# Optimization experiments

Hardware: AMD Instinct MI355X
Metric: run time of the kernel (lower is better)

Reference implementation:

```python
import jax, jax.numpy as jnp
import numpy as np
import math

B, T, C, H = 4, 2048, 768, 12
D = C // H  # 64 head dim

def setup_inputs() -> dict:
    key = jax.random.key(0)
    k1, k2, k3 = jax.random.split(key, 3)
    x = jax.random.normal(k1, (B, T, C), dtype=jnp.float32)
    mask = jnp.tril(jnp.ones((T, T), dtype=bool))[None, None, :, :]  # causal [1,1,T,T]
    W_attn = jax.random.normal(k2, (C, 3 * C), dtype=jnp.float32) * 0.02
    b_attn = jnp.zeros((3 * C,), dtype=jnp.float32)
    W_proj = jax.random.normal(k3, (C, C), dtype=jnp.float32) * (0.02 / math.sqrt(2 * 12))
    b_proj = jnp.zeros((C,), dtype=jnp.float32)
    return {"x": x, "mask": mask, "W_attn": W_attn, "b_attn": b_attn,
            "W_proj": W_proj, "b_proj": b_proj}

def reference(x, mask, W_attn, b_attn, W_proj, b_proj):
    Bx, Tx, Cx = x.shape
    qkv = x @ W_attn + b_attn                       # [B,T,3C]
    qkv = qkv.reshape(Bx, Tx, 3 * H, D).transpose(0, 2, 1, 3)  # [B,3H,T,D]
    q, k, v = jnp.array_split(qkv, 3, axis=1)       # each [B,H,T,D]
    att = jnp.einsum('bhqd,bhkd->bhqk', q, k) / math.sqrt(D)  # [B,H,T,T]
    att = jnp.where(mask == 0, -jnp.inf, att)
    att = jax.nn.softmax(att, axis=-1)
    y = jnp.einsum('bhqk,bhkd->bhqd', att, v)       # [B,H,T,D]
    y = y.transpose(0, 2, 1, 3).reshape(Bx, Tx, Cx)
    return y @ W_proj + b_proj
```

## Files before the change

kernel.cpp:

```cpp
#include <hip/hip_runtime.h>
#include <math.h>

#define BB 4
#define TT 2048
#define CC 768
#define HH 12
#define DD 64
#define RS (3 * CC)

typedef __bf16 bf16x8 __attribute__((ext_vector_type(8)));
typedef float f32x4 __attribute__((ext_vector_type(4)));
typedef unsigned short u16x8 __attribute__((ext_vector_type(8)));

union U8 { bf16x8 v; u16x8 s; unsigned short u[8]; };
union BCV { __bf16 h; unsigned short u; };

__device__ __forceinline__ unsigned short f2bf(float f) {
  union { float f; unsigned u; } x; x.f = f;
  unsigned r = x.u + 0x7fffu + ((x.u >> 16) & 1u);
  return (unsigned short)(r >> 16);
}

#define AS1 __attribute__((address_space(1)))
#define AS3 __attribute__((address_space(3)))
__device__ __forceinline__ void gl_lds16(const void* g, void* l) {
  __builtin_amdgcn_global_load_lds((const AS1 unsigned int*)g,
                                   (AS3 unsigned int*)l, 16, 0, 0);
}

__global__ __launch_bounds__(256) void cvt_bf16_kernel(
    const float* __restrict__ in, unsigned short* __restrict__ out, int n8) {
  int i = blockIdx.x * 256 + threadIdx.x;
  const int stride = gridDim.x * 256;
  for (; i < n8; i += stride) {
    const float4 a = reinterpret_cast<const float4*>(in)[i * 2];
    const float4 b = reinterpret_cast<const float4*>(in)[i * 2 + 1];
    U8 p;
    p.u[0] = f2bf(a.x); p.u[1] = f2bf(a.y); p.u[2] = f2bf(a.z); p.u[3] = f2bf(a.w);
    p.u[4] = f2bf(b.x); p.u[5] = f2bf(b.y); p.u[6] = f2bf(b.z); p.u[7] = f2bf(b.w);
    reinterpret_cast<u16x8*>(out)[i] = p.s;
  }
}

__global__ __launch_bounds__(256) void transpose_cvt_kernel(
    const float* __restrict__ in, unsigned short* __restrict__ out,
    int K, int N) {
  __shared__ float T[64][65];
  const int k0 = blockIdx.y * 64, n0 = blockIdx.x * 64;
  const int tid = threadIdx.x;
  const int ty = tid >> 4, tx4 = (tid & 15) * 4;
#pragma unroll
  for (int i = 0; i < 4; ++i) {
    const int r = ty + i * 16;
    const float4 v = *reinterpret_cast<const float4*>(
        &in[(size_t)(k0 + r) * N + n0 + tx4]);
    T[r][tx4] = v.x; T[r][tx4 + 1] = v.y; T[r][tx4 + 2] = v.z; T[r][tx4 + 3] = v.w;
  }
  __syncthreads();
  const int nrow = tid >> 2, kc = (tid & 3) * 16;
  U8 p0, p1;
#pragma unroll
  for (int i = 0; i < 8; ++i) {
    p0.u[i] = f2bf(T[kc + i][nrow]);
    p1.u[i] = f2bf(T[kc + 8 + i][nrow]);
  }
  unsigned short* o = &out[(size_t)(n0 + nrow) * K + k0 + kc];
  *reinterpret_cast<u16x8*>(o) = p0.s;
  *reinterpret_cast<u16x8*>(o + 8) = p1.s;
}

__global__ __launch_bounds__(256) void vtrans_kernel(
    const unsigned short* __restrict__ qkvb, unsigned short* __restrict__ Vg) {
  __shared__ unsigned short Tt[64][72];
  const int tok0 = blockIdx.x * 64;
  const int bh = blockIdx.y, b = bh / HH, h = bh % HH;
  const int tid = threadIdx.x;
  const int r = tid >> 2, c = (tid & 3) * 16;
  const unsigned short* src =
      qkvb + (size_t)(b * TT + tok0 + r) * RS + (2 * HH + h) * DD + c;
  *reinterpret_cast<u16x8*>(&Tt[r][c]) = *reinterpret_cast<const u16x8*>(src);
  *reinterpret_cast<u16x8*>(&Tt[r][c + 8]) =
      *reinterpret_cast<const u16x8*>(src + 8);
  __syncthreads();
  const int d = tid >> 2, tc = (tid & 3) * 16;
  U8 o0, o1;
#pragma unroll
  for (int i = 0; i < 8; ++i) {
    o0.u[i] = Tt[tc + i][d];
    o1.u[i] = Tt[tc + 8 + i][d];
  }
  unsigned short* dst = Vg + ((size_t)bh * DD + d) * TT + tok0 + tc;
  *reinterpret_cast<u16x8*>(dst) = o0.s;
  *reinterpret_cast<u16x8*>(dst + 8) = o1.s;
}

template <typename OutT>
__global__ __launch_bounds__(256) void gemm_mfma_kernel(
    const unsigned short* __restrict__ A, const unsigned short* __restrict__ Bt,
    const float* __restrict__ bias, OutT* __restrict__ C,
    int M, int N, int K) {
  __shared__ unsigned short As[128 * 32];
  __shared__ unsigned short Bs[128 * 32];

  const int tid = threadIdx.x;
  const int w = tid >> 6, l = tid & 63, lr = l & 15, lg = l >> 4;
  const int wr = w >> 1, wc = w & 1;
  const int brow = blockIdx.y * 128, bcol = blockIdx.x * 128;

  f32x4 acc[4][4];
#pragma unroll
  for (int i = 0; i < 4; ++i)
#pragma unroll
    for (int j = 0; j < 4; ++j) acc[i][j] = (f32x4)(0.f);

  const int r0 = tid >> 2, c8 = (tid & 3) * 8;
  const unsigned short* gA = A + (size_t)(brow + r0) * K + c8;
  const unsigned short* gB = Bt + (size_t)(bcol + r0) * K + c8;
  unsigned short* lA = As + w * 512;
  unsigned short* lB = Bs + w * 512;

  for (int k0 = 0; k0 < K; k0 += 32) {
    __syncthreads();
    gl_lds16(gA + k0, lA);
    gl_lds16(gA + (size_t)64 * K + k0, lA + 2048);
    gl_lds16(gB + k0, lB);
    gl_lds16(gB + (size_t)64 * K + k0, lB + 2048);
    __syncthreads();

    bf16x8 af[4], bf[4];
#pragma unroll
    for (int mf = 0; mf < 4; ++mf)
      af[mf] = *reinterpret_cast<const bf16x8*>(
          &As[(wr * 64 + mf * 16 + lr) * 32 + lg * 8]);
#pragma unroll
    for (int nf = 0; nf < 4; ++nf)
      bf[nf] = *reinterpret_cast<const bf16x8*>(
          &Bs[(wc * 64 + nf * 16 + lr) * 32 + lg * 8]);
#pragma unroll
    for (int mf = 0; mf < 4; ++mf)
#pragma unroll
      for (int nf = 0; nf < 4; ++nf)
        acc[mf][nf] = __builtin_amdgcn_mfma_f32_16x16x32_bf16(
            af[mf], bf[nf], acc[mf][nf], 0, 0, 0);
  }

#pragma unroll
  for (int nf = 0; nf < 4; ++nf) {
    const int col = bcol + wc * 64 + nf * 16 + lr;
    const float bv = bias[col];
#pragma unroll
    for (int mf = 0; mf < 4; ++mf) {
      const int row0 = brow + wr * 64 + mf * 16 + lg * 4;
#pragma unroll
      for (int r = 0; r < 4; ++r) {
        const float v = acc[mf][nf][r] + bv;
        if constexpr (sizeof(OutT) == 2)
          C[(size_t)(row0 + r) * N + col] = (OutT)f2bf(v);
        else
          C[(size_t)(row0 + r) * N + col] = (OutT)v;
      }
    }
  }
}

constexpr int KVT = 64;

__global__ __launch_bounds__(256) void attn_mfma_kernel(
    const unsigned short* __restrict__ qkv,
    const unsigned short* __restrict__ Vg,
    unsigned short* __restrict__ y) {
  __shared__ unsigned short Ks[KVT * 64];
  __shared__ unsigned short Vt[DD * 64];
  __shared__ unsigned short Pl[4 * 16 * 64];

  const int tid = threadIdx.x;
  const int w = tid >> 6, l = tid & 63;
  const int lr = l & 15, lg = l >> 4;
  const int bh = blockIdx.x, b = bh / HH, h = bh % HH;
  const int g = 31 - blockIdx.y;
  const int qw = g * 64 + w * 16;

  const unsigned short* qbase = qkv + (size_t)b * TT * RS + h * DD;
  const unsigned short* kbase = qkv + (size_t)b * TT * RS + (HH + h) * DD;
  const unsigned short* vgb = Vg + (size_t)bh * DD * TT;

  const float qscale = 0.125f * 1.44269504f;
  const int e = lg ^ (lr & 7);
  const int e4 = e ^ 4;

  bf16x8 qf[2];
  {
    const unsigned short* qrow = qbase + (size_t)(qw + lr) * RS;
    qf[0] = *reinterpret_cast<const bf16x8*>(qrow + lg * 8);
    qf[1] = *reinterpret_cast<const bf16x8*>(qrow + lg * 8 + 32);
  }

  f32x4 O[4];
  f32x4 ls = (f32x4)(0.f);
#pragma unroll
  for (int nb = 0; nb < 4; ++nb) O[nb] = (f32x4)(0.f);

  const int srow = tid >> 2, sc2 = (tid & 3) * 2;
  const int sw = srow & 7;
  const int sidx0 = srow * 64 + 8 * (sc2 ^ sw);
  const int sidx1 = srow * 64 + 8 * ((sc2 + 1) ^ sw);
  const int scol = (tid & 3) * 16;
  const unsigned short* kptr = kbase + (size_t)srow * RS + scol;
  const unsigned short* vptr = vgb + (size_t)srow * TT + scol;

  const int ntiles = g + 1;
  u16x8 kr0 = *reinterpret_cast<const u16x8*>(kptr);
  u16x8 kr1 = *reinterpret_cast<const u16x8*>(kptr + 8);
  u16x8 vr0 = *reinterpret_cast<const u16x8*>(vptr);
  u16x8 vr1 = *reinterpret_cast<const u16x8*>(vptr + 8);

  for (int t = 0; t < ntiles; ++t) {
    const int kv0 = t * KVT;
    __syncthreads();
    *reinterpret_cast<u16x8*>(&Ks[sidx0]) = kr0;
    *reinterpret_cast<u16x8*>(&Ks[sidx1]) = kr1;
    *reinterpret_cast<u16x8*>(&Vt[sidx0]) = vr0;
    *reinterpret_cast<u16x8*>(&Vt[sidx1]) = vr1;
    if (t + 1 < ntiles) {
      kptr += (size_t)KVT * RS;
      vptr += KVT;
      kr0 = *reinterpret_cast<const u16x8*>(kptr);
      kr1 = *reinterpret_cast<const u16x8*>(kptr + 8);
      vr0 = *reinterpret_cast<const u16x8*>(vptr);
      vr1 = *reinterpret_cast<const u16x8*>(vptr + 8);
    }
    __syncthreads();

    const bool diag = (t == g);
    const int nbmax = diag ? (w + 1) : 4;

    f32x4 s[4];
#pragma unroll
    for (int nb = 0; nb < 4; ++nb) s[nb] = (f32x4)(0.f);
#pragma unroll
    for (int nb = 0; nb < 4; ++nb) {
      if (nb >= nbmax) continue;
      const int krow = (nb * 16 + lr) * 64;
      const bf16x8 k0 = *reinterpret_cast<const bf16x8*>(&Ks[krow + 8 * e]);
      const bf16x8 k1 = *reinterpret_cast<const bf16x8*>(&Ks[krow + 8 * e4]);
      s[nb] = __builtin_amdgcn_mfma_f32_16x16x32_bf16(qf[0], k0, s[nb], 0, 0, 0);
      s[nb] = __builtin_amdgcn_mfma_f32_16x16x32_bf16(qf[1], k1, s[nb], 0, 0, 0);
    }

#pragma unroll
    for (int nb = 0; nb < 4; ++nb)
#pragma unroll
      for (int r = 0; r < 4; ++r) s[nb][r] *= qscale;
    if (diag) {
      const int qrow = qw + lg * 4;
#pragma unroll
      for (int nb = 0; nb < 4; ++nb) {
        const int key = kv0 + nb * 16 + lr;
#pragma unroll
        for (int r = 0; r < 4; ++r)
          if (key > qrow + r) s[nb][r] = -1e30f;
      }
    }
#pragma unroll
    for (int r = 0; r < 4; ++r) {
      const int prow = lg * 4 + r;
      const int pswz = (prow & 7) << 3;
      unsigned short* pbase = &Pl[w * 1024 + prow * 64];
#pragma unroll
      for (int nb = 0; nb < 4; ++nb) {
        const float p = exp2f(s[nb][r]);
        ls[r] += p;
        BCV cv; cv.h = (__bf16)p;
        pbase[(nb * 16 + lr) ^ pswz] = cv.u;
      }
    }

    asm volatile("s_waitcnt lgkmcnt(0)" ::: "memory");

    {
      const unsigned short* pw = &Pl[w * 1024];
      const bf16x8 pa0 = *reinterpret_cast<const bf16x8*>(&pw[lr * 64 + 8 * e]);
      const bf16x8 pa1 = *reinterpret_cast<const bf16x8*>(&pw[lr * 64 + 8 * e4]);
#pragma unroll
      for (int nb = 0; nb < 4; ++nb) {
        const int vrow = (nb * 16 + lr) * 64;
        const bf16x8 v0 = *reinterpret_cast<const bf16x8*>(&Vt[vrow + 8 * e]);
        const bf16x8 v1 = *reinterpret_cast<const bf16x8*>(&Vt[vrow + 8 * e4]);
        O[nb] = __builtin_amdgcn_mfma_f32_16x16x32_bf16(pa0, v0, O[nb], 0, 0, 0);
        O[nb] = __builtin_amdgcn_mfma_f32_16x16x32_bf16(pa1, v1, O[nb], 0, 0, 0);
      }
    }
  }

#pragma unroll
  for (int off = 1; off < 16; off <<= 1)
#pragma unroll
    for (int r = 0; r < 4; ++r) ls[r] += __shfl_xor(ls[r], off, 64);
  f32x4 inv;
#pragma unroll
  for (int r = 0; r < 4; ++r) inv[r] = 1.f / ls[r];
#pragma unroll
  for (int nb = 0; nb < 4; ++nb)
#pragma unroll
    for (int r = 0; r < 4; ++r)
      y[((size_t)b * TT + qw + lg * 4 + r) * CC + h * DD + nb * 16 + lr] =
          f2bf(O[nb][r] * inv[r]);
}

extern "C" void kernel_launch(void* const* d_in, const int* in_sizes, int n_in,
                              void* d_out, int out_size, void* d_ws, size_t ws_size,
                              hipStream_t stream) {
  const float* x      = (const float*)d_in[0];
  const float* W_attn = (const float*)d_in[2];
  const float* b_attn = (const float*)d_in[3];
  const float* W_proj = (const float*)d_in[4];
  const float* b_proj = (const float*)d_in[5];
  float* out = (float*)d_out;

  const int M = BB * TT;
  unsigned short* qkvb = (unsigned short*)d_ws;
  unsigned short* xb   = qkvb + (size_t)M * RS;
  unsigned short* yb   = xb + (size_t)M * CC;
  unsigned short* Wt1  = yb + (size_t)M * CC;
  unsigned short* Wt2  = Wt1 + (size_t)RS * CC;
  unsigned short* Vg   = xb;

  cvt_bf16_kernel<<<1024, 256, 0, stream>>>(x, xb, M * CC / 8);
  transpose_cvt_kernel<<<dim3(RS / 64, CC / 64), 256, 0, stream>>>(
      W_attn, Wt1, CC, RS);
  transpose_cvt_kernel<<<dim3(CC / 64, CC / 64), 256, 0, stream>>>(
      W_proj, Wt2, CC, CC);

  gemm_mfma_kernel<unsigned short><<<dim3(RS / 128, M / 128), 256, 0, stream>>>(
      xb, Wt1, b_attn, qkvb, M, RS, CC);

  vtrans_kernel<<<dim3(TT / 64, BB * HH), 256, 0, stream>>>(qkvb, Vg);

  attn_mfma_kernel<<<dim3(BB * HH, 32), 256, 0, stream>>>(qkvb, Vg, yb);

  gemm_mfma_kernel<float><<<dim3(CC / 128, M / 128), 256, 0, stream>>>(
      yb, Wt2, b_proj, out, M, CC, CC);
}
```

Measured before the change: 154.5 us.

## Double-buffer LDS tiles in GEMM and attention kernels, one barrier per iteration

Both the GEMM and the attention kernel now use two LDS buffers. The next K/V or A/B tile is written into the spare buffer while MFMAs consume the current one, which cuts the barriers per loop iteration from two to one. The aim is to overlap global-to-LDS staging with compute and reduce synchronisation stalls. The cost is double the LDS footprint, which may lower occupancy.

```diff
diff --git a/kernel.cpp b/kernel.cpp
--- a/kernel.cpp
+++ b/kernel.cpp
@@ -99,8 +99,8 @@
     const unsigned short* __restrict__ A, const unsigned short* __restrict__ Bt,
     const float* __restrict__ bias, OutT* __restrict__ C,
     int M, int N, int K) {
-  __shared__ unsigned short As[128 * 32];
-  __shared__ unsigned short Bs[128 * 32];
+  __shared__ unsigned short As[2][128 * 32];
+  __shared__ unsigned short Bs[2][128 * 32];
 
   const int tid = threadIdx.x;
   const int w = tid >> 6, l = tid & 63, lr = l & 15, lg = l >> 4;
@@ -116,32 +116,41 @@
   const int r0 = tid >> 2, c8 = (tid & 3) * 8;
   const unsigned short* gA = A + (size_t)(brow + r0) * K + c8;
   const unsigned short* gB = Bt + (size_t)(bcol + r0) * K + c8;
-  unsigned short* lA = As + w * 512;
-  unsigned short* lB = Bs + w * 512;
-
+
+  gl_lds16(gA, As[0] + w * 512);
+  gl_lds16(gA + (size_t)64 * K, As[0] + w * 512 + 2048);
+  gl_lds16(gB, Bs[0] + w * 512);
+  gl_lds16(gB + (size_t)64 * K, Bs[0] + w * 512 + 2048);
+  __syncthreads();
+
+  int cur = 0;
   for (int k0 = 0; k0 < K; k0 += 32) {
-    __syncthreads();
-    gl_lds16(gA + k0, lA);
-    gl_lds16(gA + (size_t)64 * K + k0, lA + 2048);
-    gl_lds16(gB + k0, lB);
-    gl_lds16(gB + (size_t)64 * K + k0, lB + 2048);
-    __syncthreads();
+    if (k0 + 32 < K) {
+      const int kn = k0 + 32;
+      gl_lds16(gA + kn, As[cur ^ 1] + w * 512);
+      gl_lds16(gA + (size_t)64 * K + kn, As[cur ^ 1] + w * 512 + 2048);
+      gl_lds16(gB + kn, Bs[cur ^ 1] + w * 512);
+      gl_lds16(gB + (size_t)64 * K + kn, Bs[cur ^ 1] + w * 512 + 2048);
+    }
 
     bf16x8 af[4], bf[4];
 #pragma unroll
     for (int mf = 0; mf < 4; ++mf)
       af[mf] = *reinterpret_cast<const bf16x8*>(
-          &As[(wr * 64 + mf * 16 + lr) * 32 + lg * 8]);
+          &As[cur][(wr * 64 + mf * 16 + lr) * 32 + lg * 8]);
 #pragma unroll
     for (int nf = 0; nf < 4; ++nf)
       bf[nf] = *reinterpret_cast<const bf16x8*>(
-          &Bs[(wc * 64 + nf * 16 + lr) * 32 + lg * 8]);
+          &Bs[cur][(wc * 64 + nf * 16 + lr) * 32 + lg * 8]);
 #pragma unroll
     for (int mf = 0; mf < 4; ++mf)
 #pragma unroll
       for (int nf = 0; nf < 4; ++nf)
         acc[mf][nf] = __builtin_amdgcn_mfma_f32_16x16x32_bf16(
             af[mf], bf[nf], acc[mf][nf], 0, 0, 0);
+
+    __syncthreads();
+    cur ^= 1;
   }
 
 #pragma unroll
@@ -169,8 +178,8 @@
     const unsigned short* __restrict__ qkv,
     const unsigned short* __restrict__ Vg,
     unsigned short* __restrict__ y) {
-  __shared__ unsigned short Ks[KVT * 64];
-  __shared__ unsigned short Vt[DD * 64];
+  __shared__ unsigned short Ks[2][KVT * 64];
+  __shared__ unsigned short Vt[2][DD * 64];
   __shared__ unsigned short Pl[4 * 16 * 64];
 
   const int tid = threadIdx.x;
@@ -214,22 +223,38 @@
   u16x8 vr0 = *reinterpret_cast<const u16x8*>(vptr);
   u16x8 vr1 = *reinterpret_cast<const u16x8*>(vptr + 8);
 
+  *reinterpret_cast<u16x8*>(&Ks[0][sidx0]) = kr0;
+  *reinterpret_cast<u16x8*>(&Ks[0][sidx1]) = kr1;
+  *reinterpret_cast<u16x8*>(&Vt[0][sidx0]) = vr0;
+  *reinterpret_cast<u16x8*>(&Vt[0][sidx1]) = vr1;
+  if (ntiles > 1) {
+    kptr += (size_t)KVT * RS;
+    vptr += KVT;
+    kr0 = *reinterpret_cast<const u16x8*>(kptr);
+    kr1 = *reinterpret_cast<const u16x8*>(kptr + 8);
+    vr0 = *reinterpret_cast<const u16x8*>(vptr);
+    vr1 = *reinterpret_cast<const u16x8*>(vptr + 8);
+  }
+  __syncthreads();
+
+  int cur = 0;
   for (int t = 0; t < ntiles; ++t) {
     const int kv0 = t * KVT;
-    __syncthreads();
-    *reinterpret_cast<u16x8*>(&Ks[sidx0]) = kr0;
-    *reinterpret_cast<u16x8*>(&Ks[sidx1]) = kr1;
-    *reinterpret_cast<u16x8*>(&Vt[sidx0]) = vr0;
-    *reinterpret_cast<u16x8*>(&Vt[sidx1]) = vr1;
+
     if (t + 1 < ntiles) {
-      kptr += (size_t)KVT * RS;
-      vptr += KVT;
-      kr0 = *reinterpret_cast<const u16x8*>(kptr);
-      kr1 = *reinterpret_cast<const u16x8*>(kptr + 8);
-      vr0 = *reinterpret_cast<const u16x8*>(vptr);
-      vr1 = *reinterpret_cast<const u16x8*>(vptr + 8);
-    }
-    __syncthreads();
+      *reinterpret_cast<u16x8*>(&Ks[cur ^ 1][sidx0]) = kr0;
+      *reinterpret_cast<u16x8*>(&Ks[cur ^ 1][sidx1]) = kr1;
+      *reinterpret_cast<u16x8*>(&Vt[cur ^ 1][sidx0]) = vr0;
+      *reinterpret_cast<u16x8*>(&Vt[cur ^ 1][sidx1]) = vr1;
+      if (t + 2 < ntiles) {
+        kptr += (size_t)KVT * RS;
+        vptr += KVT;
+        kr0 = *reinterpret_cast<const u16x8*>(kptr);
+        kr1 = *reinterpret_cast<const u16x8*>(kptr + 8);
+        vr0 = *reinterpret_cast<const u16x8*>(vptr);
+        vr1 = *reinterpret_cast<const u16x8*>(vptr + 8);
+      }
+    }
 
     const bool diag = (t == g);
     const int nbmax = diag ? (w + 1) : 4;
@@ -241,8 +266,8 @@
     for (int nb = 0; nb < 4; ++nb) {
       if (nb >= nbmax) continue;
       const int krow = (nb * 16 + lr) * 64;
-      const bf16x8 k0 = *reinterpret_cast<const bf16x8*>(&Ks[krow + 8 * e]);
-      const bf16x8 k1 = *reinterpret_cast<const bf16x8*>(&Ks[krow + 8 * e4]);
+      const bf16x8 k0 = *reinterpret_cast<const bf16x8*>(&Ks[cur][krow + 8 * e]);
+      const bf16x8 k1 = *reinterpret_cast<const bf16x8*>(&Ks[cur][krow + 8 * e4]);
       s[nb] = __builtin_amdgcn_mfma_f32_16x16x32_bf16(qf[0], k0, s[nb], 0, 0, 0);
       s[nb] = __builtin_amdgcn_mfma_f32_16x16x32_bf16(qf[1], k1, s[nb], 0, 0, 0);
     }
@@ -284,12 +309,15 @@
 #pragma unroll
       for (int nb = 0; nb < 4; ++nb) {
         const int vrow = (nb * 16 + lr) * 64;
-        const bf16x8 v0 = *reinterpret_cast<const bf16x8*>(&Vt[vrow + 8 * e]);
-        const bf16x8 v1 = *reinterpret_cast<const bf16x8*>(&Vt[vrow + 8 * e4]);
+        const bf16x8 v0 = *reinterpret_cast<const bf16x8*>(&Vt[cur][vrow + 8 * e]);
+        const bf16x8 v1 = *reinterpret_cast<const bf16x8*>(&Vt[cur][vrow + 8 * e4]);
         O[nb] = __builtin_amdgcn_mfma_f32_16x16x32_bf16(pa0, v0, O[nb], 0, 0, 0);
         O[nb] = __builtin_amdgcn_mfma_f32_16x16x32_bf16(pa1, v1, O[nb], 0, 0, 0);
       }
     }
+
+    __syncthreads();
+    cur ^= 1;
   }
 
 #pragma unroll
```

Result: slower. 158.2 us (+2.4%).

## Double-buffer GEMM LDS tiles and trim masked softmax work in attention

Applied to the files above, without the earlier changes.

The GEMM kernel now keeps two LDS buffers and issues the global-to-LDS loads for the next K slice before running the MFMAs on the current one, so each iteration needs one barrier instead of two. In the attention kernel the qscale multiply is folded into the exp2 argument and masked-out key blocks on the diagonal tile skip exp2, writing zeros instead. s_setprio raises wave priority around the MFMA sections. LDS use in the GEMM doubles, which can lower occupancy.

```diff
diff --git a/kernel.cpp b/kernel.cpp
--- a/kernel.cpp
+++ b/kernel.cpp
@@ -99,8 +99,8 @@
     const unsigned short* __restrict__ A, const unsigned short* __restrict__ Bt,
     const float* __restrict__ bias, OutT* __restrict__ C,
     int M, int N, int K) {
-  __shared__ unsigned short As[128 * 32];
-  __shared__ unsigned short Bs[128 * 32];
+  __shared__ unsigned short As[2][128 * 32];
+  __shared__ unsigned short Bs[2][128 * 32];
 
   const int tid = threadIdx.x;
   const int w = tid >> 6, l = tid & 63, lr = l & 15, lg = l >> 4;
@@ -116,32 +116,41 @@
   const int r0 = tid >> 2, c8 = (tid & 3) * 8;
   const unsigned short* gA = A + (size_t)(brow + r0) * K + c8;
   const unsigned short* gB = Bt + (size_t)(bcol + r0) * K + c8;
-  unsigned short* lA = As + w * 512;
-  unsigned short* lB = Bs + w * 512;
-
+
+  gl_lds16(gA, As[0] + w * 512);
+  gl_lds16(gA + (size_t)64 * K, As[0] + w * 512 + 2048);
+  gl_lds16(gB, Bs[0] + w * 512);
+  gl_lds16(gB + (size_t)64 * K, Bs[0] + w * 512 + 2048);
+  __syncthreads();
+
+  int cur = 0;
   for (int k0 = 0; k0 < K; k0 += 32) {
-    __syncthreads();
-    gl_lds16(gA + k0, lA);
-    gl_lds16(gA + (size_t)64 * K + k0, lA + 2048);
-    gl_lds16(gB + k0, lB);
-    gl_lds16(gB + (size_t)64 * K + k0, lB + 2048);
-    __syncthreads();
+    if (k0 + 32 < K) {
+      const int kn = k0 + 32;
+      gl_lds16(gA + kn, As[cur ^ 1] + w * 512);
+      gl_lds16(gA + (size_t)64 * K + kn, As[cur ^ 1] + w * 512 + 2048);
+      gl_lds16(gB + kn, Bs[cur ^ 1] + w * 512);
+      gl_lds16(gB + (size_t)64 * K + kn, Bs[cur ^ 1] + w * 512 + 2048);
+    }
 
     bf16x8 af[4], bf[4];
 #pragma unroll
     for (int mf = 0; mf < 4; ++mf)
       af[mf] = *reinterpret_cast<const bf16x8*>(
-          &As[(wr * 64 + mf * 16 + lr) * 32 + lg * 8]);
+          &As[cur][(wr * 64 + mf * 16 + lr) * 32 + lg * 8]);
 #pragma unroll
     for (int nf = 0; nf < 4; ++nf)
       bf[nf] = *reinterpret_cast<const bf16x8*>(
-          &Bs[(wc * 64 + nf * 16 + lr) * 32 + lg * 8]);
+          &Bs[cur][(wc * 64 + nf * 16 + lr) * 32 + lg * 8]);
 #pragma unroll
     for (int mf = 0; mf < 4; ++mf)
 #pragma unroll
       for (int nf = 0; nf < 4; ++nf)
         acc[mf][nf] = __builtin_amdgcn_mfma_f32_16x16x32_bf16(
             af[mf], bf[nf], acc[mf][nf], 0, 0, 0);
+
+    __syncthreads();
+    cur ^= 1;
   }
 
 #pragma unroll
@@ -237,6 +246,7 @@
     f32x4 s[4];
 #pragma unroll
     for (int nb = 0; nb < 4; ++nb) s[nb] = (f32x4)(0.f);
+    __builtin_amdgcn_s_setprio(1);
 #pragma unroll
     for (int nb = 0; nb < 4; ++nb) {
       if (nb >= nbmax) continue;
@@ -246,15 +256,13 @@
       s[nb] = __builtin_amdgcn_mfma_f32_16x16x32_bf16(qf[0], k0, s[nb], 0, 0, 0);
       s[nb] = __builtin_amdgcn_mfma_f32_16x16x32_bf16(qf[1], k1, s[nb], 0, 0, 0);
     }
-
-#pragma unroll
-    for (int nb = 0; nb < 4; ++nb)
-#pragma unroll
-      for (int r = 0; r < 4; ++r) s[nb][r] *= qscale;
+    __builtin_amdgcn_s_setprio(0);
+
     if (diag) {
       const int qrow = qw + lg * 4;
 #pragma unroll
       for (int nb = 0; nb < 4; ++nb) {
+        if (nb >= nbmax) continue;
         const int key = kv0 + nb * 16 + lr;
 #pragma unroll
         for (int r = 0; r < 4; ++r)
@@ -268,7 +276,11 @@
       unsigned short* pbase = &Pl[w * 1024 + prow * 64];
 #pragma unroll
       for (int nb = 0; nb < 4; ++nb) {
-        const float p = exp2f(s[nb][r]);
+        if (nb >= nbmax) {
+          pbase[(nb * 16 + lr) ^ pswz] = 0;
+          continue;
+        }
+        const float p = exp2f(s[nb][r] * qscale);
         ls[r] += p;
         BCV cv; cv.h = (__bf16)p;
         pbase[(nb * 16 + lr) ^ pswz] = cv.u;
@@ -281,6 +293,7 @@
       const unsigned short* pw = &Pl[w * 1024];
       const bf16x8 pa0 = *reinterpret_cast<const bf16x8*>(&pw[lr * 64 + 8 * e]);
       const bf16x8 pa1 = *reinterpret_cast<const bf16x8*>(&pw[lr * 64 + 8 * e4]);
+      __builtin_amdgcn_s_setprio(1);
 #pragma unroll
       for (int nb = 0; nb < 4; ++nb) {
         const int vrow = (nb * 16 + lr) * 64;
@@ -289,6 +302,7 @@
         O[nb] = __builtin_amdgcn_mfma_f32_16x16x32_bf16(pa0, v0, O[nb], 0, 0, 0);
         O[nb] = __builtin_amdgcn_mfma_f32_16x16x32_bf16(pa1, v1, O[nb], 0, 0, 0);
       }
+      __builtin_amdgcn_s_setprio(0);
     }
   }
 
```

Result: faster. 151.4 us (-2.0%).
